# Performance work log

Measured on AMD Instinct MI355X. Metric: run time of the kernel, lower is better.

## Reference

```python
import jax, jax.numpy as jnp
import numpy as np

B, C = 32768, 4096

def setup_inputs() -> dict:
    key = jax.random.key(0)
    k1, k2, k3 = jax.random.split(key, 3)
    output = jax.random.normal(k1, (B, C), dtype=jnp.float32)
    target = jax.random.randint(k2, (B,), 0, C, dtype=jnp.int64)
    # dense per-(true, pred) error weight matrix; torch dict lookup == gather here
    weights = jax.random.uniform(k3, (C, C), dtype=jnp.float32, minval=0.5, maxval=2.0)
    return {"output": output, "target": target, "weights": weights}

def reference(output, target, weights):
    # per-sample cross entropy (reduction='none')
    logp = jax.nn.log_softmax(output, axis=-1)            # [B, C]
    ce = -jnp.take_along_axis(logp, target[:, None], axis=-1)[:, 0]  # [B]
    pred = jnp.argmax(output, axis=-1)                    # [B]
    w = weights[target, pred]                             # gather per (true, pred)
    return jnp.mean(ce * w)
```

## Files before the change

### kernel.cpp

```cpp
#include <hip/hip_runtime.h>


#define NROWS 32768
#define NCOLS 4096

typedef float f32x4 __attribute__((ext_vector_type(4)));

__global__ __launch_bounds__(256) void wl_rows_kernel(
    const float* __restrict__ logits,
    const int* __restrict__ target,
    const float* __restrict__ weights,
    float* __restrict__ partial) {
  const int wave = threadIdx.x >> 6;
  const int lane = threadIdx.x & 63;
  const int row = blockIdx.x * 4 + wave;
  const float* rowp = logits + (size_t)row * NCOLS;

  const int t = target[row];
  const int tchunk = t >> 2;
  const int tlane = tchunk & 63;
  const int tit = tchunk >> 6;
  const int tcomp = t & 3;

  f32x4 v[16];
#pragma unroll
  for (int it = 0; it < 16; ++it) {
    v[it] = __builtin_nontemporal_load(
        reinterpret_cast<const f32x4*>(rowp + it * 256 + lane * 4));
  }

  float cand = 0.f;
#pragma unroll
  for (int it = 0; it < 16; ++it) {
    if (it == tit) {
      const float a = (tcomp & 1) ? v[it].y : v[it].x;
      const float b = (tcomp & 1) ? v[it].w : v[it].z;
      cand = (tcomp & 2) ? b : a;
    }
  }
  const float xt = __shfl(cand, tlane, 64);

  float bv = v[0].x;
  int bi = lane * 4;
#pragma unroll
  for (int it = 0; it < 16; ++it) {
    const int base = it * 256 + lane * 4;
    if (v[it].x > bv) { bv = v[it].x; bi = base + 0; }
    if (v[it].y > bv) { bv = v[it].y; bi = base + 1; }
    if (v[it].z > bv) { bv = v[it].z; bi = base + 2; }
    if (v[it].w > bv) { bv = v[it].w; bi = base + 3; }
  }

#pragma unroll
  for (int off = 32; off > 0; off >>= 1) {
    float ov = __shfl_xor(bv, off, 64);
    int oi = __shfl_xor(bi, off, 64);
    if (ov > bv || (ov == bv && oi < bi)) { bv = ov; bi = oi; }
  }

  float s = 0.f;
#pragma unroll
  for (int it = 0; it < 16; ++it) {
    s += __expf(v[it].x - bv);
    s += __expf(v[it].y - bv);
    s += __expf(v[it].z - bv);
    s += __expf(v[it].w - bv);
  }
#pragma unroll
  for (int off = 32; off > 0; off >>= 1) {
    s += __shfl_xor(s, off, 64);
  }

  if (lane == 0) {
    const float w = weights[(size_t)t * NCOLS + bi];
    const float ce = bv + __logf(s) - xt;
    partial[row] = ce * w;
  }
}

__global__ __launch_bounds__(1024) void wl_reduce_kernel(
    const float* __restrict__ partial, float* __restrict__ out) {
  __shared__ float wsum[16];
  const int tid = threadIdx.x;
  float s = 0.f;
  const f32x4* p4 = reinterpret_cast<const f32x4*>(partial);
#pragma unroll
  for (int i = 0; i < 8; ++i) {
    f32x4 p = p4[tid + i * 1024];
    s += p.x + p.y + p.z + p.w;
  }
#pragma unroll
  for (int off = 32; off > 0; off >>= 1) s += __shfl_xor(s, off, 64);
  if ((tid & 63) == 0) wsum[tid >> 6] = s;
  __syncthreads();
  if (tid < 16) {
    s = wsum[tid];
#pragma unroll
    for (int off = 8; off > 0; off >>= 1) s += __shfl_xor(s, off, 64);
    if (tid == 0) out[0] = s * (1.0f / NROWS);
  }
}

extern "C" void kernel_launch(void* const* d_in, const int* in_sizes, int n_in,
                              void* d_out, int out_size, void* d_ws, size_t ws_size,
                              hipStream_t stream) {
  const float* logits = (const float*)d_in[0];
  const int* target = (const int*)d_in[1];
  const float* weights = (const float*)d_in[2];
  float* partial = (float*)d_ws;
  float* out = (float*)d_out;

  wl_rows_kernel<<<NROWS / 4, 256, 0, stream>>>(logits, target, weights, partial);
  wl_reduce_kernel<<<1, 1024, 0, stream>>>(partial, out);
}
```

Before: 676.2 us.

## Process one row per 256-thread block with cross-wave LDS reductions

```diff
diff --git a/kernel.cpp b/kernel.cpp
--- a/kernel.cpp
+++ b/kernel.cpp
@@ -11,69 +11,87 @@
     const int* __restrict__ target,
     const float* __restrict__ weights,
     float* __restrict__ partial) {
-  const int wave = threadIdx.x >> 6;
-  const int lane = threadIdx.x & 63;
-  const int row = blockIdx.x * 4 + wave;
+  const int tid = threadIdx.x;
+  const int lane = tid & 63;
+  const int wid = tid >> 6;
+  const int row = blockIdx.x;
   const float* rowp = logits + (size_t)row * NCOLS;
+
+  __shared__ float ls_val[4];
+  __shared__ int ls_idx[4];
+  __shared__ float ls_sum[4];
+  __shared__ float ls_xt;
 
   const int t = target[row];
   const int tchunk = t >> 2;
-  const int tlane = tchunk & 63;
-  const int tit = tchunk >> 6;
+  const int towner = tchunk & 255;
+  const int tit = tchunk >> 8;
   const int tcomp = t & 3;
 
-  f32x4 v[16];
+  f32x4 v[4];
 #pragma unroll
-  for (int it = 0; it < 16; ++it) {
+  for (int it = 0; it < 4; ++it) {
     v[it] = __builtin_nontemporal_load(
-        reinterpret_cast<const f32x4*>(rowp + it * 256 + lane * 4));
+        reinterpret_cast<const f32x4*>(rowp + (it * 256 + tid) * 4));
   }
 
-  float cand = 0.f;
+  if (tid == towner) {
+    float cand = 0.f;
 #pragma unroll
-  for (int it = 0; it < 16; ++it) {
-    if (it == tit) {
-      const float a = (tcomp & 1) ? v[it].y : v[it].x;
-      const float b = (tcomp & 1) ? v[it].w : v[it].z;
-      cand = (tcomp & 2) ? b : a;
+    for (int it = 0; it < 4; ++it) {
+      if (it == tit) {
+        const float a = (tcomp & 1) ? v[it].y : v[it].x;
+        const float b = (tcomp & 1) ? v[it].w : v[it].z;
+        cand = (tcomp & 2) ? b : a;
+      }
     }
+    ls_xt = cand;
   }
-  const float xt = __shfl(cand, tlane, 64);
 
   float bv = v[0].x;
-  int bi = lane * 4;
+  int bi = tid * 4;
 #pragma unroll
-  for (int it = 0; it < 16; ++it) {
-    const int base = it * 256 + lane * 4;
+  for (int it = 0; it < 4; ++it) {
+    const int base = (it * 256 + tid) * 4;
     if (v[it].x > bv) { bv = v[it].x; bi = base + 0; }
     if (v[it].y > bv) { bv = v[it].y; bi = base + 1; }
     if (v[it].z > bv) { bv = v[it].z; bi = base + 2; }
     if (v[it].w > bv) { bv = v[it].w; bi = base + 3; }
   }
-
 #pragma unroll
   for (int off = 32; off > 0; off >>= 1) {
     float ov = __shfl_xor(bv, off, 64);
     int oi = __shfl_xor(bi, off, 64);
     if (ov > bv || (ov == bv && oi < bi)) { bv = ov; bi = oi; }
   }
+  if (lane == 0) { ls_val[wid] = bv; ls_idx[wid] = bi; }
+  __syncthreads();
+  bv = ls_val[0];
+  bi = ls_idx[0];
+#pragma unroll
+  for (int w = 1; w < 4; ++w) {
+    const float ov = ls_val[w];
+    const int oi = ls_idx[w];
+    if (ov > bv || (ov == bv && oi < bi)) { bv = ov; bi = oi; }
+  }
 
   float s = 0.f;
 #pragma unroll
-  for (int it = 0; it < 16; ++it) {
+  for (int it = 0; it < 4; ++it) {
     s += __expf(v[it].x - bv);
     s += __expf(v[it].y - bv);
     s += __expf(v[it].z - bv);
     s += __expf(v[it].w - bv);
   }
 #pragma unroll
-  for (int off = 32; off > 0; off >>= 1) {
-    s += __shfl_xor(s, off, 64);
-  }
+  for (int off = 32; off > 0; off >>= 1) s += __shfl_xor(s, off, 64);
+  if (lane == 0) ls_sum[wid] = s;
+  __syncthreads();
 
-  if (lane == 0) {
+  if (tid == 0) {
+    const float st = ls_sum[0] + ls_sum[1] + ls_sum[2] + ls_sum[3];
     const float w = weights[(size_t)t * NCOLS + bi];
-    const float ce = bv + __logf(s) - xt;
+    const float ce = bv + __logf(st) - ls_xt;
     partial[row] = ce * w;
   }
 }
@@ -110,6 +128,6 @@
   float* partial = (float*)d_ws;
   float* out = (float*)d_out;
 
-  wl_rows_kernel<<<NROWS / 4, 256, 0, stream>>>(logits, target, weights, partial);
+  wl_rows_kernel<<<NROWS, 256, 0, stream>>>(logits, target, weights, partial);
   wl_reduce_kernel<<<1, 1024, 0, stream>>>(partial, out);
 }
```

Measured after the change: 676.4 us. Within noise of the previous version (+0.0%).
